# Kernel tuning notes

Measured on AMD Instinct MI355X. Metric: run time of the kernel, lower is better.

The kernel has to match this reference:

```python
import jax, jax.numpy as jnp
import numpy as np
import math

N_EMBD = 1024
N_HEAD = 16
HEAD_SIZE = N_EMBD // N_HEAD
LAYER_IDX = 2
LAMBDA_INIT = 0.8 - 0.6 * math.exp(-0.3 * (LAYER_IDX - 1))
LN_EPS = 1e-5
B, T = 4, 1024


def setup_inputs() -> dict:
    key = jax.random.key(0)
    ks = jax.random.split(key, 11)
    s = 0.02  # weight init scale
    return {
        "x": jax.random.normal(ks[0], (B, T, N_EMBD), dtype=jnp.float32),
        "Wq1": jax.random.normal(ks[1], (N_EMBD, N_EMBD), dtype=jnp.float32) * s,
        "Wq2": jax.random.normal(ks[2], (N_EMBD, N_EMBD), dtype=jnp.float32) * s,
        "Wk1": jax.random.normal(ks[3], (N_EMBD, N_EMBD), dtype=jnp.float32) * s,
        "Wk2": jax.random.normal(ks[4], (N_EMBD, N_EMBD), dtype=jnp.float32) * s,
        "Wv": jax.random.normal(ks[5], (N_EMBD, 2 * N_EMBD), dtype=jnp.float32) * s,
        "Wc": jax.random.normal(ks[6], (2 * N_EMBD, N_EMBD), dtype=jnp.float32) * s,
        "lq1": jax.random.normal(ks[7], (N_HEAD, HEAD_SIZE), dtype=jnp.float32) * 0.1,
        "lk1": jax.random.normal(ks[8], (N_HEAD, HEAD_SIZE), dtype=jnp.float32) * 0.1,
        "lq2": jax.random.normal(ks[9], (N_HEAD, HEAD_SIZE), dtype=jnp.float32) * 0.1,
        "lk2": jax.random.normal(ks[10], (N_HEAD, HEAD_SIZE), dtype=jnp.float32) * 0.1,
    }


def reference(x, Wq1, Wq2, Wk1, Wk2, Wv, Wc, lq1, lk1, lq2, lk2):
    Bx, Tx, C = x.shape
    H, hs = N_HEAD, HEAD_SIZE
    scale = 1.0 / math.sqrt(hs)

    # projections -> (B, T, H, d)
    q1 = (x @ Wq1).reshape(Bx, Tx, H, hs)
    q2 = (x @ Wq2).reshape(Bx, Tx, H, hs)
    k1 = (x @ Wk1).reshape(Bx, Tx, H, hs)
    k2 = (x @ Wk2).reshape(Bx, Tx, H, hs)
    v = (x @ Wv).reshape(Bx, Tx, H, 2 * hs)

    # dual score streams (B, H, T, T)
    att1 = jnp.einsum("bqhd,bkhd->bhqk", q1, k1) * scale
    att2 = jnp.einsum("bqhd,bkhd->bhqk", q2, k2) * scale

    causal = jnp.tril(jnp.ones((Tx, Tx), dtype=bool))  # (T, T)
    neg_inf = jnp.float32(-jnp.inf)
    att1 = jnp.where(causal, att1, neg_inf)
    att2 = jnp.where(causal, att2, neg_inf)
    a1 = jax.nn.softmax(att1, axis=-1)
    a2 = jax.nn.softmax(att2, axis=-1)

    # per-head differential lambda
    lam1 = jnp.exp(jnp.sum(lq1 * lk1, axis=-1))  # (H,)
    lam2 = jnp.exp(jnp.sum(lq2 * lk2, axis=-1))  # (H,)
    lam_full = lam1 - lam2 + LAMBDA_INIT  # (H,)

    att = a1 - lam_full[None, :, None, None] * a2  # dropout = identity (eval)

    # PV matmul -> (B, T, H, 2*hs)
    y = jnp.einsum("bhqk,bkhd->bqhd", att, v)

    # subLN over last dim (no affine)
    mu = jnp.mean(y, axis=-1, keepdims=True)
    var = jnp.mean(jnp.square(y - mu), axis=-1, keepdims=True)
    y = (y - mu) / jnp.sqrt(var + LN_EPS)
    y = y * (1.0 - LAMBDA_INIT)

    y = y.reshape(Bx, Tx, 2 * C)
    return y @ Wc  # resid dropout = identity (eval)
```

## Files before the change

kernel.cpp:

```cpp
#include <hip/hip_runtime.h>


#define T_SEQ 1024
#define NH 16
#define DV 128
#define NPROJ 6144
#define KSTR 72

typedef __bf16 bf16_t;
typedef __bf16 bf16x8 __attribute__((ext_vector_type(8)));
typedef __bf16 bf16x4 __attribute__((ext_vector_type(4)));
typedef short s16x4 __attribute__((ext_vector_type(4)));
typedef float f32x4 __attribute__((ext_vector_type(4)));

#define LAMBDA_INIT 0.35550906759096928f
#define ONE_MINUS_LI 0.6444909324090307f
#define LOG2E 1.4426950408889634f

#if __has_builtin(__builtin_amdgcn_mfma_f32_16x16x16_bf16)
#define MFMA16(a, b, c) __builtin_amdgcn_mfma_f32_16x16x16_bf16(a, b, c, 0, 0, 0)
#elif __has_builtin(__builtin_amdgcn_mfma_f32_16x16x16bf16_1k)
#define MFMA16(a, b, c)                                                       \
  __builtin_amdgcn_mfma_f32_16x16x16bf16_1k(                                  \
      __builtin_bit_cast(s16x4, a), __builtin_bit_cast(s16x4, b), c, 0, 0, 0)
#else
#define MFMA16(a, b, c) (c)
#endif

#define GLDS(g, l)                                                            \
  __builtin_amdgcn_global_load_lds(                                           \
      (const __attribute__((address_space(1))) void*)(g),                     \
      (__attribute__((address_space(3))) void*)(l), 16, 0, 0)

static const size_t OFF_WCAT = 0;
static const size_t OFF_XB = OFF_WCAT + (size_t)6144 * 1024 * 2;
static const size_t OFF_WCT = OFF_XB + (size_t)4096 * 1024 * 2;
static const size_t OFF_PROJ = OFF_WCT + (size_t)2048 * 1024 * 2;
static const size_t OFF_VT = OFF_PROJ + (size_t)4096 * 6144 * 2;
static const size_t OFF_YLN = OFF_VT + (size_t)64 * 128 * 1024 * 2;
static const size_t OFF_LAM = OFF_YLN + (size_t)4096 * 2048 * 2;

__global__ void __launch_bounds__(256) cast_x(const float* __restrict__ x,
                                              bf16_t* __restrict__ o) {
  const int i = (blockIdx.x * 256 + threadIdx.x) * 4;
  float4 v = *(const float4*)(x + i);
  bf16x4 r = {(bf16_t)v.x, (bf16_t)v.y, (bf16_t)v.z, (bf16_t)v.w};
  *(bf16x4*)(o + i) = r;
}

__device__ __forceinline__ void tcast_body(const float* __restrict__ W,
                                           bf16_t* __restrict__ Wt, int K,
                                           int N, int row0) {
  __shared__ float tile[32][33];
  const int k0 = blockIdx.x * 32, n0 = blockIdx.y * 32;
  const int tx = threadIdx.x & 31, ty = threadIdx.x >> 5;
#pragma unroll
  for (int i = 0; i < 32; i += 8)
    tile[ty + i][tx] = W[(long)(k0 + ty + i) * N + n0 + tx];
  __syncthreads();
#pragma unroll
  for (int i = 0; i < 32; i += 8)
    Wt[(long)(row0 + n0 + ty + i) * K + k0 + tx] = (bf16_t)tile[tx][ty + i];
}

__global__ void __launch_bounds__(256) tcast_w(const float* __restrict__ W,
                                               bf16_t* __restrict__ Wt, int K,
                                               int N, int row0) {
  tcast_body(W, Wt, K, N, row0);
}

__global__ void __launch_bounds__(256) tcast_w4(const float* __restrict__ W0,
                                                const float* __restrict__ W1,
                                                const float* __restrict__ W2,
                                                const float* __restrict__ W3,
                                                bf16_t* __restrict__ Wt) {
  const float* Ws[4] = {W0, W1, W2, W3};
  tcast_body(Ws[blockIdx.z], Wt, 1024, 1024, blockIdx.z * 1024);
}

__global__ void lam_kernel(const float* __restrict__ lq1,
                           const float* __restrict__ lk1,
                           const float* __restrict__ lq2,
                           const float* __restrict__ lk2,
                           float* __restrict__ lam) {
  const int h = threadIdx.x;
  if (h < NH) {
    float d1 = 0.f, d2 = 0.f;
    for (int i = 0; i < 64; ++i) {
      d1 += lq1[h * 64 + i] * lk1[h * 64 + i];
      d2 += lq2[h * 64 + i] * lk2[h * 64 + i];
    }
    lam[h] = expf(d1) - expf(d2) + LAMBDA_INIT;
  }
}

#define BM 128
#define BN 128
#define BK 32

template <typename OutT>
__global__ void __launch_bounds__(256) gemm_bt(const bf16_t* __restrict__ A,
                                               const bf16_t* __restrict__ Bt,
                                               OutT* __restrict__ C, int M,
                                               int N, int K) {
  __shared__ __align__(16) bf16_t As[BM * BK];
  __shared__ __align__(16) bf16_t Bs[BN * BK];
  const int tid = threadIdx.x;
  const int w = tid >> 6;
  const int lane = tid & 63;
  const int quad = lane >> 4, l16 = lane & 15;
  const int m0 = blockIdx.y * BM, n0 = blockIdx.x * BN;
  const int wm = (w >> 1) * 64, wn = (w & 1) * 64;
  const int srow = tid >> 2;
  const int scol = (tid & 3) * 8;

  const bf16_t* Ag0 = A + (long)(m0 + srow) * K + scol;
  const bf16_t* Ag1 = Ag0 + (long)64 * K;
  const bf16_t* Bg0 = Bt + (long)(n0 + srow) * K + scol;
  const bf16_t* Bg1 = Bg0 + (long)64 * K;
  bf16_t* lA0 = As + tid * 8;
  bf16_t* lA1 = As + 2048 + tid * 8;
  bf16_t* lB0 = Bs + tid * 8;
  bf16_t* lB1 = Bs + 2048 + tid * 8;

  f32x4 acc[4][4] = {};

  for (int k0 = 0; k0 < K; k0 += BK) {
    GLDS(Ag0 + k0, lA0);
    GLDS(Ag1 + k0, lA1);
    GLDS(Bg0 + k0, lB0);
    GLDS(Bg1 + k0, lB1);
    __syncthreads();
    bf16x8 af[4], bfr[4];
#pragma unroll
    for (int t = 0; t < 4; ++t) {
      af[t] = *(const bf16x8*)(As + (wm + t * 16 + l16) * BK + quad * 8);
      bfr[t] = *(const bf16x8*)(Bs + (wn + t * 16 + l16) * BK + quad * 8);
    }
#pragma unroll
    for (int mt = 0; mt < 4; ++mt)
#pragma unroll
      for (int nt = 0; nt < 4; ++nt)
        acc[mt][nt] = __builtin_amdgcn_mfma_f32_16x16x32_bf16(
            af[mt], bfr[nt], acc[mt][nt], 0, 0, 0);
    __syncthreads();
  }

#pragma unroll
  for (int mt = 0; mt < 4; ++mt)
#pragma unroll
    for (int nt = 0; nt < 4; ++nt) {
      const int col = n0 + wn + nt * 16 + l16;
#pragma unroll
      for (int i = 0; i < 4; ++i) {
        const int row = m0 + wm + mt * 16 + quad * 4 + i;
        C[(long)row * N + col] = (OutT)acc[mt][nt][i];
      }
    }
}

__global__ void __launch_bounds__(256) transpose_v(const bf16_t* __restrict__ proj,
                                                   bf16_t* __restrict__ vt) {
  __shared__ bf16_t tile[32][34];
  const int bh = blockIdx.z;
  const int b = bh >> 4, h = bh & 15;
  const int t0 = blockIdx.x * 32, d0 = blockIdx.y * 32;
  const int tx = threadIdx.x & 31, ty = threadIdx.x >> 5;
  const bf16_t* src = proj + (long)(b * T_SEQ) * NPROJ + 4096 + h * 128;
#pragma unroll
  for (int i = 0; i < 32; i += 8)
    tile[ty + i][tx] = src[(long)(t0 + ty + i) * NPROJ + d0 + tx];
  __syncthreads();
  bf16_t* dst = vt + ((long)(b * NH + h) * DV) * T_SEQ;
#pragma unroll
  for (int i = 0; i < 32; i += 8)
    dst[(long)(d0 + ty + i) * T_SEQ + t0 + tx] = tile[tx][ty + i];
}

__global__ void __launch_bounds__(256) attn_kernel(const bf16_t* __restrict__ proj,
                                                   const bf16_t* __restrict__ vt,
                                                   const float* __restrict__ lamp,
                                                   bf16_t* __restrict__ yln) {
  const int p = blockIdx.x >> 4;
  const int h = blockIdx.x & 15;
  const int b = blockIdx.y;
  const int tid = threadIdx.x;
  const int w = tid >> 6, lane = tid & 63;
  const int quad = lane >> 4, l16 = lane & 15;
  const long bT = (long)b * T_SEQ;

  __shared__ __align__(16) bf16_t Ks1[64 * KSTR];
  __shared__ __align__(16) bf16_t Ks2[64 * KSTR];
  __shared__ __align__(16) bf16_t Vs[DV * KSTR];

  const bf16_t* gK1 =
      proj + (bT + (tid >> 3)) * (long)NPROJ + h * 64 + 2048 + (tid & 7) * 8;
  const bf16_t* gK2 = gK1 + 1024;
  const bf16_t* vbase = vt + ((long)(b * NH + h) * DV) * T_SEQ;
  const bf16_t* gV = vbase + (long)(tid >> 3) * T_SEQ + (tid & 7) * 8;
  const int kw0 = (tid >> 3) * KSTR + (tid & 7) * 8;

  const float sc = 0.125f * LOG2E;
  const float lam = lamp[h];

  for (int phase = 0; phase < 2; ++phase) {
    const int qblk = phase == 0 ? (15 - p) : p;
    const int q0 = qblk * 64 + w * 16;
    const int qg = q0 + l16;

    const bf16_t* qrow = proj + (bT + qg) * (long)NPROJ + h * 64;
    bf16x8 aq1[2], aq2[2];
    aq1[0] = *(const bf16x8*)(qrow + quad * 8);
    aq1[1] = *(const bf16x8*)(qrow + 32 + quad * 8);
    aq2[0] = *(const bf16x8*)(qrow + 1024 + quad * 8);
    aq2[1] = *(const bf16x8*)(qrow + 1024 + 32 + quad * 8);

    f32x4 O1[8] = {}, O2[8] = {};
    float m1 = -3.0e38f, m2 = -3.0e38f, l1 = 0.f, l2 = 0.f;

    const int kend_blk = qblk * 64 + 64;
    const int kend_w = q0 + 16;

    bf16x8 rK1[2], rK2[2], rV[4];
    rK1[0] = *(const bf16x8*)(gK1);
    rK1[1] = *(const bf16x8*)(gK1 + (long)32 * NPROJ);
    rK2[0] = *(const bf16x8*)(gK2);
    rK2[1] = *(const bf16x8*)(gK2 + (long)32 * NPROJ);
#pragma unroll
    for (int j = 0; j < 4; ++j)
      rV[j] = *(const bf16x8*)(gV + (long)(32 * j) * T_SEQ);

    for (int kt = 0; kt < kend_blk; kt += 64) {
      *(bf16x8*)(Ks1 + kw0) = rK1[0];
      *(bf16x8*)(Ks1 + kw0 + 32 * KSTR) = rK1[1];
      *(bf16x8*)(Ks2 + kw0) = rK2[0];
      *(bf16x8*)(Ks2 + kw0 + 32 * KSTR) = rK2[1];
#pragma unroll
      for (int j = 0; j < 4; ++j)
        *(bf16x8*)(Vs + kw0 + j * 32 * KSTR) = rV[j];
      __syncthreads();

      if (kt + 64 < kend_blk) {
        const long ko = (long)(kt + 64) * NPROJ;
        rK1[0] = *(const bf16x8*)(gK1 + ko);
        rK1[1] = *(const bf16x8*)(gK1 + ko + (long)32 * NPROJ);
        rK2[0] = *(const bf16x8*)(gK2 + ko);
        rK2[1] = *(const bf16x8*)(gK2 + ko + (long)32 * NPROJ);
#pragma unroll
        for (int j = 0; j < 4; ++j)
          rV[j] = *(const bf16x8*)(gV + kt + 64 + (long)(32 * j) * T_SEQ);
      }

      if (kt < kend_w) {
        f32x4 s1[4], s2[4];
#pragma unroll
        for (int c = 0; c < 4; ++c) {
          const bf16_t* kr1 = Ks1 + (c * 16 + l16) * KSTR;
          const bf16_t* kr2 = Ks2 + (c * 16 + l16) * KSTR;
          bf16x8 ka0 = *(const bf16x8*)(kr1 + quad * 8);
          bf16x8 ka1 = *(const bf16x8*)(kr1 + 32 + quad * 8);
          f32x4 z = {};
          z = __builtin_amdgcn_mfma_f32_16x16x32_bf16(ka0, aq1[0], z, 0, 0, 0);
          z = __builtin_amdgcn_mfma_f32_16x16x32_bf16(ka1, aq1[1], z, 0, 0, 0);
          s1[c] = z;
          bf16x8 kb0 = *(const bf16x8*)(kr2 + quad * 8);
          bf16x8 kb1 = *(const bf16x8*)(kr2 + 32 + quad * 8);
          f32x4 z2 = {};
          z2 = __builtin_amdgcn_mfma_f32_16x16x32_bf16(kb0, aq2[0], z2, 0, 0, 0);
          z2 = __builtin_amdgcn_mfma_f32_16x16x32_bf16(kb1, aq2[1], z2, 0, 0, 0);
          s2[c] = z2;
        }
        const bool need_mask = (kt + 63 > q0);
        float mx1 = -3.0e38f, mx2 = -3.0e38f;
#pragma unroll
        for (int c = 0; c < 4; ++c) {
#pragma unroll
          for (int i = 0; i < 4; ++i) {
            const int key = kt + c * 16 + quad * 4 + i;
            float v1 = s1[c][i] * sc, v2 = s2[c][i] * sc;
            if (need_mask && key > qg) {
              v1 = -1e30f;
              v2 = -1e30f;
            }
            s1[c][i] = v1;
            s2[c][i] = v2;
            mx1 = fmaxf(mx1, v1);
            mx2 = fmaxf(mx2, v2);
          }
        }
        mx1 = fmaxf(mx1, __shfl_xor(mx1, 16));
        mx1 = fmaxf(mx1, __shfl_xor(mx1, 32));
        mx2 = fmaxf(mx2, __shfl_xor(mx2, 16));
        mx2 = fmaxf(mx2, __shfl_xor(mx2, 32));
        const float mn1 = fmaxf(m1, mx1), mn2 = fmaxf(m2, mx2);
        const float al1 = exp2f(m1 - mn1), al2 = exp2f(m2 - mn2);
        m1 = mn1;
        m2 = mn2;
        bf16x4 pc1[4], pc2[4];
        float sum1 = 0.f, sum2 = 0.f;
#pragma unroll
        for (int c = 0; c < 4; ++c) {
#pragma unroll
          for (int i = 0; i < 4; ++i) {
            bf16_t p1 = (bf16_t)exp2f(s1[c][i] - m1);
            bf16_t p2 = (bf16_t)exp2f(s2[c][i] - m2);
            pc1[c][i] = p1;
            pc2[c][i] = p2;
            sum1 += (float)p1;
            sum2 += (float)p2;
          }
        }
        sum1 += __shfl_xor(sum1, 16);
        sum1 += __shfl_xor(sum1, 32);
        sum2 += __shfl_xor(sum2, 16);
        sum2 += __shfl_xor(sum2, 32);
        l1 = l1 * al1 + sum1;
        l2 = l2 * al2 + sum2;
#pragma unroll
        for (int f = 0; f < 8; ++f)
#pragma unroll
          for (int i = 0; i < 4; ++i) {
            O1[f][i] *= al1;
            O2[f][i] *= al2;
          }
#pragma unroll
        for (int c = 0; c < 4; ++c) {
#pragma unroll
          for (int f = 0; f < 8; ++f) {
            bf16x4 va =
                *(const bf16x4*)(Vs + (f * 16 + l16) * KSTR + c * 16 + quad * 4);
            O1[f] = MFMA16(va, pc1[c], O1[f]);
            O2[f] = MFMA16(va, pc2[c], O2[f]);
          }
        }
      }
      __syncthreads();
    }

    const float inv1 = 1.0f / l1, inv2 = lam / l2;
    float sm = 0.f, sq = 0.f;
#pragma unroll
    for (int f = 0; f < 8; ++f)
#pragma unroll
      for (int i = 0; i < 4; ++i) {
        float y = O1[f][i] * inv1 - O2[f][i] * inv2;
        O1[f][i] = y;
        sm += y;
        sq += y * y;
      }
    sm += __shfl_xor(sm, 16);
    sm += __shfl_xor(sm, 32);
    sq += __shfl_xor(sq, 16);
    sq += __shfl_xor(sq, 32);
    const float mu = sm * (1.0f / 128.0f);
    const float var = sq * (1.0f / 128.0f) - mu * mu;
    const float rs = rsqrtf(var + 1e-5f) * ONE_MINUS_LI;
    bf16_t* dst = yln + (bT + qg) * (long)2048 + h * 128 + quad * 4;
#pragma unroll
    for (int f = 0; f < 8; ++f) {
      bf16x4 o = {(bf16_t)((O1[f][0] - mu) * rs), (bf16_t)((O1[f][1] - mu) * rs),
                  (bf16_t)((O1[f][2] - mu) * rs), (bf16_t)((O1[f][3] - mu) * rs)};
      *(bf16x4*)(dst + f * 16) = o;
    }
  }
}

extern "C" void kernel_launch(void* const* d_in, const int* in_sizes, int n_in,
                              void* d_out, int out_size, void* d_ws,
                              size_t ws_size, hipStream_t stream) {
  const float* x = (const float*)d_in[0];
  const float* Wq1 = (const float*)d_in[1];
  const float* Wq2 = (const float*)d_in[2];
  const float* Wk1 = (const float*)d_in[3];
  const float* Wk2 = (const float*)d_in[4];
  const float* Wv = (const float*)d_in[5];
  const float* Wc = (const float*)d_in[6];
  const float* lq1 = (const float*)d_in[7];
  const float* lk1 = (const float*)d_in[8];
  const float* lq2 = (const float*)d_in[9];
  const float* lk2 = (const float*)d_in[10];
  float* out = (float*)d_out;

  char* ws = (char*)d_ws;
  bf16_t* wcat = (bf16_t*)(ws + OFF_WCAT);
  bf16_t* xb = (bf16_t*)(ws + OFF_XB);
  bf16_t* wct = (bf16_t*)(ws + OFF_WCT);
  bf16_t* projb = (bf16_t*)(ws + OFF_PROJ);
  bf16_t* vtb = (bf16_t*)(ws + OFF_VT);
  bf16_t* ylnb = (bf16_t*)(ws + OFF_YLN);
  float* lamp = (float*)(ws + OFF_LAM);

  cast_x<<<4096, 256, 0, stream>>>(x, xb);
  tcast_w4<<<dim3(32, 32, 4), 256, 0, stream>>>(Wq1, Wq2, Wk1, Wk2, wcat);
  tcast_w<<<dim3(32, 64), 256, 0, stream>>>(Wv, wcat, 1024, 2048, 4096);
  tcast_w<<<dim3(64, 32), 256, 0, stream>>>(Wc, wct, 2048, 1024, 0);
  lam_kernel<<<1, 64, 0, stream>>>(lq1, lk1, lq2, lk2, lamp);

  gemm_bt<bf16_t><<<dim3(48, 32), 256, 0, stream>>>(xb, wcat, projb, 4096, 6144, 1024);
  transpose_v<<<dim3(32, 4, 64), 256, 0, stream>>>(projb, vtb);
  attn_kernel<<<dim3(128, 4), 256, 0, stream>>>(projb, vtb, lamp, ylnb);
  gemm_bt<float><<<dim3(8, 32), 256, 0, stream>>>(ylnb, wct, out, 4096, 1024, 2048);
}
```

Measured before the change: 333.3 us.

## Split attention into one block per query tile, add lazy rescale and MFMA row sums

The attention grid changes from 512 blocks, each handling a paired long and short query tile, to 1024 blocks with one 64-row query tile each, ordered longest first. Score scaling moves into a single fma inside the exp. Rescaling of the running max is skipped when the new max stays within a threshold, a FlashAttention-4-style lazy rescale. Row sums are computed with an MFMA against a ones vector instead of shuffles. This adds parallelism and removes VALU and shuffle work, but the bf16 P sums and the skip threshold could affect numerics.

```diff
diff --git a/kernel.cpp b/kernel.cpp
--- a/kernel.cpp
+++ b/kernel.cpp
@@ -16,6 +16,7 @@
 #define LAMBDA_INIT 0.35550906759096928f
 #define ONE_MINUS_LI 0.6444909324090307f
 #define LOG2E 1.4426950408889634f
+#define RTHR 44.36f
 
 #if __has_builtin(__builtin_amdgcn_mfma_f32_16x16x16_bf16)
 #define MFMA16(a, b, c) __builtin_amdgcn_mfma_f32_16x16x16_bf16(a, b, c, 0, 0, 0)
@@ -181,9 +182,10 @@
                                                    const bf16_t* __restrict__ vt,
                                                    const float* __restrict__ lamp,
                                                    bf16_t* __restrict__ yln) {
-  const int p = blockIdx.x >> 4;
-  const int h = blockIdx.x & 15;
-  const int b = blockIdx.y;
+  const int x = blockIdx.x;
+  const int qblk = 15 - (x >> 6);
+  const int bh = x & 63;
+  const int b = bh >> 4, h = bh & 15;
   const int tid = threadIdx.x;
   const int w = tid >> 6, lane = tid & 63;
   const int quad = lane >> 4, l16 = lane & 15;
@@ -203,119 +205,104 @@
   const float sc = 0.125f * LOG2E;
   const float lam = lamp[h];
 
-  for (int phase = 0; phase < 2; ++phase) {
-    const int qblk = phase == 0 ? (15 - p) : p;
-    const int q0 = qblk * 64 + w * 16;
-    const int qg = q0 + l16;
-
-    const bf16_t* qrow = proj + (bT + qg) * (long)NPROJ + h * 64;
-    bf16x8 aq1[2], aq2[2];
-    aq1[0] = *(const bf16x8*)(qrow + quad * 8);
-    aq1[1] = *(const bf16x8*)(qrow + 32 + quad * 8);
-    aq2[0] = *(const bf16x8*)(qrow + 1024 + quad * 8);
-    aq2[1] = *(const bf16x8*)(qrow + 1024 + 32 + quad * 8);
-
-    f32x4 O1[8] = {}, O2[8] = {};
-    float m1 = -3.0e38f, m2 = -3.0e38f, l1 = 0.f, l2 = 0.f;
-
-    const int kend_blk = qblk * 64 + 64;
-    const int kend_w = q0 + 16;
-
-    bf16x8 rK1[2], rK2[2], rV[4];
-    rK1[0] = *(const bf16x8*)(gK1);
-    rK1[1] = *(const bf16x8*)(gK1 + (long)32 * NPROJ);
-    rK2[0] = *(const bf16x8*)(gK2);
-    rK2[1] = *(const bf16x8*)(gK2 + (long)32 * NPROJ);
+  const int q0 = qblk * 64 + w * 16;
+  const int qg = q0 + l16;
+
+  const bf16_t* qrow = proj + (bT + qg) * (long)NPROJ + h * 64;
+  bf16x8 aq1[2], aq2[2];
+  aq1[0] = *(const bf16x8*)(qrow + quad * 8);
+  aq1[1] = *(const bf16x8*)(qrow + 32 + quad * 8);
+  aq2[0] = *(const bf16x8*)(qrow + 1024 + quad * 8);
+  aq2[1] = *(const bf16x8*)(qrow + 1024 + 32 + quad * 8);
+
+  f32x4 O1[8] = {}, O2[8] = {};
+  float m1 = -3.0e38f, m2 = -3.0e38f, l1 = 0.f, l2 = 0.f;
+
+  const int kend_blk = qblk * 64 + 64;
+  const int kend_w = q0 + 16;
+
+  const bf16x4 one4 = {(bf16_t)1.0f, (bf16_t)1.0f, (bf16_t)1.0f, (bf16_t)1.0f};
+
+  bf16x8 rK1[2], rK2[2], rV[4];
+  rK1[0] = *(const bf16x8*)(gK1);
+  rK1[1] = *(const bf16x8*)(gK1 + (long)32 * NPROJ);
+  rK2[0] = *(const bf16x8*)(gK2);
+  rK2[1] = *(const bf16x8*)(gK2 + (long)32 * NPROJ);
+#pragma unroll
+  for (int j = 0; j < 4; ++j)
+    rV[j] = *(const bf16x8*)(gV + (long)(32 * j) * T_SEQ);
+
+  for (int kt = 0; kt < kend_blk; kt += 64) {
+    *(bf16x8*)(Ks1 + kw0) = rK1[0];
+    *(bf16x8*)(Ks1 + kw0 + 32 * KSTR) = rK1[1];
+    *(bf16x8*)(Ks2 + kw0) = rK2[0];
+    *(bf16x8*)(Ks2 + kw0 + 32 * KSTR) = rK2[1];
 #pragma unroll
     for (int j = 0; j < 4; ++j)
-      rV[j] = *(const bf16x8*)(gV + (long)(32 * j) * T_SEQ);
-
-    for (int kt = 0; kt < kend_blk; kt += 64) {
-      *(bf16x8*)(Ks1 + kw0) = rK1[0];
-      *(bf16x8*)(Ks1 + kw0 + 32 * KSTR) = rK1[1];
-      *(bf16x8*)(Ks2 + kw0) = rK2[0];
-      *(bf16x8*)(Ks2 + kw0 + 32 * KSTR) = rK2[1];
+      *(bf16x8*)(Vs + kw0 + j * 32 * KSTR) = rV[j];
+    __syncthreads();
+
+    if (kt + 64 < kend_blk) {
+      const long ko = (long)(kt + 64) * NPROJ;
+      rK1[0] = *(const bf16x8*)(gK1 + ko);
+      rK1[1] = *(const bf16x8*)(gK1 + ko + (long)32 * NPROJ);
+      rK2[0] = *(const bf16x8*)(gK2 + ko);
+      rK2[1] = *(const bf16x8*)(gK2 + ko + (long)32 * NPROJ);
 #pragma unroll
       for (int j = 0; j < 4; ++j)
-        *(bf16x8*)(Vs + kw0 + j * 32 * KSTR) = rV[j];
-      __syncthreads();
-
-      if (kt + 64 < kend_blk) {
-        const long ko = (long)(kt + 64) * NPROJ;
-        rK1[0] = *(const bf16x8*)(gK1 + ko);
-        rK1[1] = *(const bf16x8*)(gK1 + ko + (long)32 * NPROJ);
-        rK2[0] = *(const bf16x8*)(gK2 + ko);
-        rK2[1] = *(const bf16x8*)(gK2 + ko + (long)32 * NPROJ);
-#pragma unroll
-        for (int j = 0; j < 4; ++j)
-          rV[j] = *(const bf16x8*)(gV + kt + 64 + (long)(32 * j) * T_SEQ);
-      }
-
-      if (kt < kend_w) {
-        f32x4 s1[4], s2[4];
-#pragma unroll
-        for (int c = 0; c < 4; ++c) {
-          const bf16_t* kr1 = Ks1 + (c * 16 + l16) * KSTR;
-          const bf16_t* kr2 = Ks2 + (c * 16 + l16) * KSTR;
-          bf16x8 ka0 = *(const bf16x8*)(kr1 + quad * 8);
-          bf16x8 ka1 = *(const bf16x8*)(kr1 + 32 + quad * 8);
-          f32x4 z = {};
-          z = __builtin_amdgcn_mfma_f32_16x16x32_bf16(ka0, aq1[0], z, 0, 0, 0);
-          z = __builtin_amdgcn_mfma_f32_16x16x32_bf16(ka1, aq1[1], z, 0, 0, 0);
-          s1[c] = z;
-          bf16x8 kb0 = *(const bf16x8*)(kr2 + quad * 8);
-          bf16x8 kb1 = *(const bf16x8*)(kr2 + 32 + quad * 8);
-          f32x4 z2 = {};
-          z2 = __builtin_amdgcn_mfma_f32_16x16x32_bf16(kb0, aq2[0], z2, 0, 0, 0);
-          z2 = __builtin_amdgcn_mfma_f32_16x16x32_bf16(kb1, aq2[1], z2, 0, 0, 0);
-          s2[c] = z2;
-        }
-        const bool need_mask = (kt + 63 > q0);
-        float mx1 = -3.0e38f, mx2 = -3.0e38f;
-#pragma unroll
-        for (int c = 0; c < 4; ++c) {
+        rV[j] = *(const bf16x8*)(gV + kt + 64 + (long)(32 * j) * T_SEQ);
+    }
+
+    if (kt < kend_w) {
+      f32x4 s1[4], s2[4];
+#pragma unroll
+      for (int c = 0; c < 4; ++c) {
+        const bf16_t* kr1 = Ks1 + (c * 16 + l16) * KSTR;
+        const bf16_t* kr2 = Ks2 + (c * 16 + l16) * KSTR;
+        bf16x8 ka0 = *(const bf16x8*)(kr1 + quad * 8);
+        bf16x8 ka1 = *(const bf16x8*)(kr1 + 32 + quad * 8);
+        f32x4 z = {};
+        z = __builtin_amdgcn_mfma_f32_16x16x32_bf16(ka0, aq1[0], z, 0, 0, 0);
+        z = __builtin_amdgcn_mfma_f32_16x16x32_bf16(ka1, aq1[1], z, 0, 0, 0);
+        s1[c] = z;
+        bf16x8 kb0 = *(const bf16x8*)(kr2 + quad * 8);
+        bf16x8 kb1 = *(const bf16x8*)(kr2 + 32 + quad * 8);
+        f32x4 z2 = {};
+        z2 = __builtin_amdgcn_mfma_f32_16x16x32_bf16(kb0, aq2[0], z2, 0, 0, 0);
+        z2 = __builtin_amdgcn_mfma_f32_16x16x32_bf16(kb1, aq2[1], z2, 0, 0, 0);
+        s2[c] = z2;
+      }
+      const bool need_mask = (kt + 63 > q0);
+      if (need_mask) {
+#pragma unroll
+        for (int c = 0; c < 4; ++c)
 #pragma unroll
           for (int i = 0; i < 4; ++i) {
             const int key = kt + c * 16 + quad * 4 + i;
-            float v1 = s1[c][i] * sc, v2 = s2[c][i] * sc;
-            if (need_mask && key > qg) {
-              v1 = -1e30f;
-              v2 = -1e30f;
+            if (key > qg) {
+              s1[c][i] = -1e30f;
+              s2[c][i] = -1e30f;
             }
-            s1[c][i] = v1;
-            s2[c][i] = v2;
-            mx1 = fmaxf(mx1, v1);
-            mx2 = fmaxf(mx2, v2);
           }
-        }
-        mx1 = fmaxf(mx1, __shfl_xor(mx1, 16));
-        mx1 = fmaxf(mx1, __shfl_xor(mx1, 32));
-        mx2 = fmaxf(mx2, __shfl_xor(mx2, 16));
-        mx2 = fmaxf(mx2, __shfl_xor(mx2, 32));
+      }
+      float t1[4], t2[4];
+#pragma unroll
+      for (int c = 0; c < 4; ++c) {
+        t1[c] = fmaxf(fmaxf(s1[c][0], s1[c][1]), fmaxf(s1[c][2], s1[c][3]));
+        t2[c] = fmaxf(fmaxf(s2[c][0], s2[c][1]), fmaxf(s2[c][2], s2[c][3]));
+      }
+      float mx1 = fmaxf(fmaxf(t1[0], t1[1]), fmaxf(t1[2], t1[3]));
+      float mx2 = fmaxf(fmaxf(t2[0], t2[1]), fmaxf(t2[2], t2[3]));
+      mx1 = fmaxf(mx1, __shfl_xor(mx1, 16));
+      mx1 = fmaxf(mx1, __shfl_xor(mx1, 32));
+      mx2 = fmaxf(mx2, __shfl_xor(mx2, 16));
+      mx2 = fmaxf(mx2, __shfl_xor(mx2, 32));
+      if (!__all((mx1 <= m1 + RTHR) && (mx2 <= m2 + RTHR))) {
         const float mn1 = fmaxf(m1, mx1), mn2 = fmaxf(m2, mx2);
-        const float al1 = exp2f(m1 - mn1), al2 = exp2f(m2 - mn2);
+        const float al1 = exp2f((m1 - mn1) * sc);
+        const float al2 = exp2f((m2 - mn2) * sc);
         m1 = mn1;
         m2 = mn2;
-        bf16x4 pc1[4], pc2[4];
-        float sum1 = 0.f, sum2 = 0.f;
-#pragma unroll
-        for (int c = 0; c < 4; ++c) {
-#pragma unroll
-          for (int i = 0; i < 4; ++i) {
-            bf16_t p1 = (bf16_t)exp2f(s1[c][i] - m1);
-            bf16_t p2 = (bf16_t)exp2f(s2[c][i] - m2);
-            pc1[c][i] = p1;
-            pc2[c][i] = p2;
-            sum1 += (float)p1;
-            sum2 += (float)p2;
-          }
-        }
-        sum1 += __shfl_xor(sum1, 16);
-        sum1 += __shfl_xor(sum1, 32);
-        sum2 += __shfl_xor(sum2, 16);
-        sum2 += __shfl_xor(sum2, 32);
-        l1 = l1 * al1 + sum1;
-        l2 = l2 * al2 + sum2;
 #pragma unroll
         for (int f = 0; f < 8; ++f)
 #pragma unroll
@@ -323,45 +310,61 @@
             O1[f][i] *= al1;
             O2[f][i] *= al2;
           }
-#pragma unroll
-        for (int c = 0; c < 4; ++c) {
-#pragma unroll
-          for (int f = 0; f < 8; ++f) {
-            bf16x4 va =
-                *(const bf16x4*)(Vs + (f * 16 + l16) * KSTR + c * 16 + quad * 4);
-            O1[f] = MFMA16(va, pc1[c], O1[f]);
-            O2[f] = MFMA16(va, pc2[c], O2[f]);
-          }
+        l1 *= al1;
+        l2 *= al2;
+      }
+      const float ms1 = m1 * sc, ms2 = m2 * sc;
+      bf16x4 pc1[4], pc2[4];
+#pragma unroll
+      for (int c = 0; c < 4; ++c)
+#pragma unroll
+        for (int i = 0; i < 4; ++i) {
+          pc1[c][i] = (bf16_t)exp2f(fmaf(s1[c][i], sc, -ms1));
+          pc2[c][i] = (bf16_t)exp2f(fmaf(s2[c][i], sc, -ms2));
         }
-      }
-      __syncthreads();
-    }
-
-    const float inv1 = 1.0f / l1, inv2 = lam / l2;
-    float sm = 0.f, sq = 0.f;
-#pragma unroll
-    for (int f = 0; f < 8; ++f)
-#pragma unroll
-      for (int i = 0; i < 4; ++i) {
-        float y = O1[f][i] * inv1 - O2[f][i] * inv2;
-        O1[f][i] = y;
-        sm += y;
-        sq += y * y;
-      }
-    sm += __shfl_xor(sm, 16);
-    sm += __shfl_xor(sm, 32);
-    sq += __shfl_xor(sq, 16);
-    sq += __shfl_xor(sq, 32);
-    const float mu = sm * (1.0f / 128.0f);
-    const float var = sq * (1.0f / 128.0f) - mu * mu;
-    const float rs = rsqrtf(var + 1e-5f) * ONE_MINUS_LI;
-    bf16_t* dst = yln + (bT + qg) * (long)2048 + h * 128 + quad * 4;
-#pragma unroll
-    for (int f = 0; f < 8; ++f) {
-      bf16x4 o = {(bf16_t)((O1[f][0] - mu) * rs), (bf16_t)((O1[f][1] - mu) * rs),
-                  (bf16_t)((O1[f][2] - mu) * rs), (bf16_t)((O1[f][3] - mu) * rs)};
-      *(bf16x4*)(dst + f * 16) = o;
-    }
+      f32x4 la1 = {}, la2 = {};
+#pragma unroll
+      for (int c = 0; c < 4; ++c) {
+        la1 = MFMA16(one4, pc1[c], la1);
+        la2 = MFMA16(one4, pc2[c], la2);
+#pragma unroll
+        for (int f = 0; f < 8; ++f) {
+          bf16x4 va =
+              *(const bf16x4*)(Vs + (f * 16 + l16) * KSTR + c * 16 + quad * 4);
+          O1[f] = MFMA16(va, pc1[c], O1[f]);
+          O2[f] = MFMA16(va, pc2[c], O2[f]);
+        }
+      }
+      l1 += la1[0];
+      l2 += la2[0];
+    }
+    __syncthreads();
+  }
+
+  const float inv1 = 1.0f / l1, inv2 = lam / l2;
+  float sm = 0.f, sq = 0.f;
+#pragma unroll
+  for (int f = 0; f < 8; ++f)
+#pragma unroll
+    for (int i = 0; i < 4; ++i) {
+      float y = O1[f][i] * inv1 - O2[f][i] * inv2;
+      O1[f][i] = y;
+      sm += y;
+      sq += y * y;
+    }
+  sm += __shfl_xor(sm, 16);
+  sm += __shfl_xor(sm, 32);
+  sq += __shfl_xor(sq, 16);
+  sq += __shfl_xor(sq, 32);
+  const float mu = sm * (1.0f / 128.0f);
+  const float var = sq * (1.0f / 128.0f) - mu * mu;
+  const float rs = rsqrtf(var + 1e-5f) * ONE_MINUS_LI;
+  bf16_t* dst = yln + (bT + qg) * (long)2048 + h * 128 + quad * 4;
+#pragma unroll
+  for (int f = 0; f < 8; ++f) {
+    bf16x4 o = {(bf16_t)((O1[f][0] - mu) * rs), (bf16_t)((O1[f][1] - mu) * rs),
+                (bf16_t)((O1[f][2] - mu) * rs), (bf16_t)((O1[f][3] - mu) * rs)};
+    *(bf16x4*)(dst + f * 16) = o;
   }
 }
 
@@ -398,6 +401,6 @@
 
   gemm_bt<bf16_t><<<dim3(48, 32), 256, 0, stream>>>(xb, wcat, projb, 4096, 6144, 1024);
   transpose_v<<<dim3(32, 4, 64), 256, 0, stream>>>(projb, vtb);
-  attn_kernel<<<dim3(128, 4), 256, 0, stream>>>(projb, vtb, lamp, ylnb);
+  attn_kernel<<<dim3(1024), 256, 0, stream>>>(projb, vtb, lamp, ylnb);
   gemm_bt<float><<<dim3(8, 32), 256, 0, stream>>>(ylnb, wct, out, 4096, 1024, 2048);
 }
```

Result: no change. 334.3 us (+0.3%).
